# Kernel optimization log

Measured on AMD Instinct MI355X. Metric: run time of the kernel, lower is better.

The kernel has to match this reference:

```python
import jax, jax.numpy as jnp
import numpy as np

B, T, C, H, DI = 4, 1024, 1024, 16, 128
TAU = 1.0
LAMBDA_CONF = 0.1
SYS2_THR = 1.0


def _ln(x, w, b):
    mu = x.mean(-1, keepdims=True)
    var = x.var(-1, keepdims=True)
    return (x - mu) * jax.lax.rsqrt(var + 1e-5) * w + b


def setup_inputs() -> dict:
    key = jax.random.key(0)
    ks = jax.random.split(key, 16)
    s = lambda i, shape: jax.random.normal(ks[i], shape, jnp.float32) * 0.02
    return {
        "h": jax.random.normal(ks[0], (B, T, C), jnp.float32),
        "ln_w": jnp.ones((C,), jnp.float32), "ln_b": jnp.zeros((C,), jnp.float32),
        "w_q": s(1, (C, C)), "w_k": s(2, (C, C)), "w_v": s(3, (C, C)),
        "w_o": s(4, (C, C)), "b_o": jnp.zeros((C,), jnp.float32),
        "U": s(5, (C, DI)), "V": s(6, (DI, C)),
        "gamma_w": s(7, (C, 1)), "gamma_b": jnp.zeros((1,), jnp.float32),
        "mass_w": s(8, (C, 1)), "mass_b": jnp.zeros((1,), jnp.float32),
        "eps_w": s(9, (C, 1)), "eps_b": jnp.zeros((1,), jnp.float32),
        "lg_w1": s(10, (C, 4 * C)), "lg_b1": jnp.zeros((4 * C,), jnp.float32),
        "lg_w2": s(11, (4 * C, C)), "lg_b2": jnp.zeros((C,), jnp.float32),
        "mlp_w1": s(12, (C, 4 * C)), "mlp_b1": jnp.zeros((4 * C,), jnp.float32),
        "mlp_w2": s(13, (4 * C, C)), "mlp_b2": jnp.zeros((C,), jnp.float32),
    }


def reference(h, ln_w, ln_b, w_q, w_k, w_v, w_o, b_o, U, V,
              gamma_w, gamma_b, mass_w, mass_b, eps_w, eps_b,
              lg_w1, lg_b1, lg_w2, lg_b2, mlp_w1, mlp_b1, mlp_w2, mlp_b2):
    hd = C // H
    h_norm = _ln(h, ln_w, ln_b)

    # ---- HamiltonianAttention (conservative force field) ----
    q = (h_norm @ w_q).reshape(B, T, H, hd).transpose(0, 2, 1, 3)  # [B,H,T,hd]
    k = (h_norm @ w_k).reshape(B, T, H, hd).transpose(0, 2, 1, 3)
    v = (h_norm @ w_v).reshape(B, T, H, hd).transpose(0, 2, 1, 3)
    scores = jnp.einsum('bhqd,bhkd->bhqk', q, k) / (hd ** 0.5) / TAU
    attn = jax.nn.softmax(scores, axis=-1)
    force = jnp.einsum('bhqk,bhkd->bhqd', attn, v).transpose(0, 2, 1, 3).reshape(B, T, C)
    f_attn = force @ w_o + b_o

    # ---- total force, low-rank projection ----
    f_total = f_attn - LAMBDA_CONF * h_norm
    f_proj = f_total @ U                               # [B,T,DI]

    # ---- FSI (force stability index) ----
    h_mag = jnp.linalg.norm(h_norm, axis=-1)           # [B,T]
    f_mag = jnp.linalg.norm(f_proj, axis=-1)
    fsi = h_mag / (2.0 * f_mag + 1e-6)

    # ---- CognitiveGearbox: per-token mass / timestep ----
    mass = 1.0 + jax.nn.softplus(h @ mass_w + mass_b)  # [B,T,1], mass >= 1
    eps = jax.nn.sigmoid(h @ eps_w + eps_b)            # [B,T,1], eps in (0,1)
    gamma = jax.nn.sigmoid(h_norm @ gamma_w + gamma_b) # [B,T,1] damping gate

    # ---- fused AGI momentum recurrence: m_t = gamma_t*m_{t-1} + (eps_t/mass_t)*f_t ----
    def step(m, inps):
        f_t, g_t, e_t, ms_t = inps                     # [B,DI],[B,1],[B,1],[B,1]
        m = g_t * m + (e_t / ms_t) * f_t
        return m, m

    xs = (f_proj.transpose(1, 0, 2), gamma.transpose(1, 0, 2),
          eps.transpose(1, 0, 2), mass.transpose(1, 0, 2))
    m0 = jnp.zeros((B, DI), h.dtype)
    _, m_seq = jax.lax.scan(step, m0, xs)              # [T,B,DI]
    m_new = m_seq.transpose(1, 0, 2)                   # [B,T,DI]

    # ---- position update + system-2 correction + MLP ----
    velocity = m_new @ V                               # [B,T,C]
    h_new = h + eps * velocity
    hn2 = _ln(h_new, ln_w, ln_b)
    sys2 = jax.nn.gelu(hn2 @ lg_w1 + lg_b1, approximate=False) @ lg_w2 + lg_b2
    gate = jax.nn.sigmoid(mass - SYS2_THR)
    h_final = h_new + gate * sys2
    hn3 = _ln(h_final, ln_w, ln_b)
    h_final = h_final + (jax.nn.gelu(hn3 @ mlp_w1 + mlp_b1, approximate=False) @ mlp_w2 + mlp_b2)
    return (h_final, m_new, fsi)
```

## Files before the change

kernel.cpp:

```cpp
#include <hip/hip_runtime.h>
#include <hip/hip_bf16.h>
#include <math.h>

typedef __attribute__((ext_vector_type(8))) short bf16x8;
typedef __attribute__((ext_vector_type(4))) float f32x4;

#define DEVI __device__ __forceinline__

constexpr int B_ = 4, T_ = 1024, C_ = 1024, H_ = 16, HD_ = 64, DI_ = 128;
constexpr int NTOK = B_ * T_;
constexpr int C4 = 4 * C_;
constexpr int C3 = 3 * C_;
constexpr float LAMBDA_CONF = 0.1f;

DEVI short f2bf(float f) {
  unsigned u = __builtin_bit_cast(unsigned, f);
  u += 0x7fffu + ((u >> 16) & 1u);
  return (short)(u >> 16);
}
DEVI unsigned pk2(float a, float b) {
  return (unsigned)(unsigned short)f2bf(a) | ((unsigned)(unsigned short)f2bf(b) << 16);
}
DEVI float sigm(float x) { return 1.f / (1.f + __expf(-x)); }
DEVI float geluf(float x) { return 0.5f * x * (1.f + erff(x * 0.70710678118654752440f)); }

DEVI void gload16(const void* g, void* l) {
  __builtin_amdgcn_global_load_lds((const __attribute__((address_space(1))) unsigned*)g,
                                   (__attribute__((address_space(3))) unsigned*)l, 16, 0, 0);
}

template <int EPI>
DEVI void epi_store(void* Outp, const float* bias, const float* resid, const float* tokv,
                    int row, int col, int N, float v) {
  size_t idx = (size_t)row * N + col;
  if (EPI == 0) {
    ((float*)Outp)[idx] = v;
  } else if (EPI == 1) {
    ((short*)Outp)[idx] = f2bf(v);
  } else if (EPI == 2) {
    ((short*)Outp)[idx] = f2bf(v + bias[col] - LAMBDA_CONF * resid[idx]);
  } else if (EPI == 3) {
    ((float*)Outp)[idx] = resid[idx] + tokv[row] * v;
  } else if (EPI == 4) {
    float x = v + bias[col];
    ((short*)Outp)[idx] = f2bf(geluf(x));
  } else if (EPI == 5) {
    float x = v + bias[col];
    float g = sigm(tokv[row] - 1.f);
    ((float*)Outp)[idx] = resid[idx] + g * x;
  } else if (EPI == 6) {
    ((float*)Outp)[idx] = resid[idx] + v + bias[col];
  }
}

__global__ __launch_bounds__(256) void transpose_cvt(const float* __restrict__ W,
                                                     short* __restrict__ Wt, int K, int N) {
  __shared__ float s[32][33];
  int n0 = blockIdx.x * 32, k0 = blockIdx.y * 32;
  int tx = threadIdx.x & 31, ty = threadIdx.x >> 5;
#pragma unroll
  for (int i = 0; i < 4; i++)
    s[ty + i * 8][tx] = W[(size_t)(k0 + ty + i * 8) * N + n0 + tx];
  __syncthreads();
#pragma unroll
  for (int i = 0; i < 4; i++)
    Wt[(size_t)(n0 + ty + i * 8) * K + k0 + tx] = f2bf(s[tx][ty + i * 8]);
}

DEVI float blk_red(float v, volatile float* sm) {
  int lane = threadIdx.x & 63, wv = threadIdx.x >> 6;
#pragma unroll
  for (int o = 32; o; o >>= 1) v += __shfl_down(v, o);
  __syncthreads();
  if (lane == 0) sm[wv] = v;
  __syncthreads();
  return sm[0] + sm[1] + sm[2] + sm[3];
}

template <int FULL, int WF32>
__global__ __launch_bounds__(256) void ln_kernel(
    const float* __restrict__ X, const float* __restrict__ lnw, const float* __restrict__ lnb,
    float* __restrict__ Out, short* __restrict__ OutBf,
    const float* __restrict__ gw, const float* __restrict__ gb,
    const float* __restrict__ mw, const float* __restrict__ mb,
    const float* __restrict__ ew, const float* __restrict__ eb,
    float* __restrict__ gammaA, float* __restrict__ epsA, float* __restrict__ massA,
    float* __restrict__ coefA, float* __restrict__ hmagA) {
  __shared__ float sm[4];
  int tok = blockIdx.x;
  const float* x = X + (size_t)tok * C_;
  int t4 = threadIdx.x * 4;
  float4 xv = *(const float4*)&x[t4];
  float s = xv.x + xv.y + xv.z + xv.w;
  float ss = xv.x * xv.x + xv.y * xv.y + xv.z * xv.z + xv.w * xv.w;
  s = blk_red(s, sm);
  ss = blk_red(ss, sm);
  float mu = s * (1.f / C_);
  float var = ss * (1.f / C_) - mu * mu;
  float rs = rsqrtf(var + 1e-5f);
  float4 wv = *(const float4*)&lnw[t4];
  float4 bv = *(const float4*)&lnb[t4];
  float4 hn;
  hn.x = (xv.x - mu) * rs * wv.x + bv.x;
  hn.y = (xv.y - mu) * rs * wv.y + bv.y;
  hn.z = (xv.z - mu) * rs * wv.z + bv.z;
  hn.w = (xv.w - mu) * rs * wv.w + bv.w;
  if (WF32) *(float4*)&Out[(size_t)tok * C_ + t4] = hn;
  short4 ob;
  ob.x = f2bf(hn.x); ob.y = f2bf(hn.y); ob.z = f2bf(hn.z); ob.w = f2bf(hn.w);
  *(short4*)&OutBf[(size_t)tok * C_ + t4] = ob;
  if (FULL) {
    float4 gwv = *(const float4*)&gw[t4];
    float4 mwv = *(const float4*)&mw[t4];
    float4 ewv = *(const float4*)&ew[t4];
    float gd = hn.x * gwv.x + hn.y * gwv.y + hn.z * gwv.z + hn.w * gwv.w;
    float md = xv.x * mwv.x + xv.y * mwv.y + xv.z * mwv.z + xv.w * mwv.w;
    float ed = xv.x * ewv.x + xv.y * ewv.y + xv.z * ewv.z + xv.w * ewv.w;
    float h2 = hn.x * hn.x + hn.y * hn.y + hn.z * hn.z + hn.w * hn.w;
    gd = blk_red(gd, sm);
    md = blk_red(md, sm);
    ed = blk_red(ed, sm);
    h2 = blk_red(h2, sm);
    if (threadIdx.x == 0) {
      float g = sigm(gd + gb[0]);
      float xm = md + mb[0];
      float sp = (xm > 20.f) ? xm : log1pf(expf(xm));
      float msv = 1.f + sp;
      float epv = sigm(ed + eb[0]);
      gammaA[tok] = g;
      massA[tok] = msv;
      epsA[tok] = epv;
      coefA[tok] = epv / msv;
      hmagA[tok] = sqrtf(h2);
    }
  }
}

template <int EPI, int MT, int NT>
__global__ __launch_bounds__(512) void gemmP(
    const short* __restrict__ A, const short* __restrict__ Bt, void* __restrict__ Outp,
    const float* __restrict__ bias, const float* __restrict__ resid,
    const float* __restrict__ tokv, int M, int N, int K) {
  constexpr int BM = 4 * MT * 16;
  constexpr int BN = 2 * NT * 16;
  constexpr int CA = BM / 64;
  constexpr int CB = BN / 64;
  constexpr int LPT = CA + CB;
  __shared__ short As[3][BM][64];
  __shared__ short Bs[3][BN][64];
  int tid = threadIdx.x, lane = tid & 63, w = tid >> 6;
  int wr = w >> 1, wc = w & 1;
  int fr = lane & 15, fg = lane >> 4;
  int nMt = M / BM;
  int cpx = gridDim.x >> 3;
  int gbid = (blockIdx.x & 7) * cpx + (blockIdx.x >> 3);
  int chunk = gbid >> 5;
  int wi = gbid & 31;
  int nCM = nMt >> 2;
  int bm = ((chunk % nCM) * 4 + (wi & 3)) * BM;
  int bn = ((chunk / nCM) * 8 + (wi >> 2)) * BN;
  f32x4 acc[MT][NT] = {};

  int jsw = (lane & 7) ^ ((lane >> 3) & 7);
  const short* gA = A + (size_t)(bm + w * 8 + (lane >> 3)) * K + (jsw << 3);
  const short* gB = Bt + (size_t)(bn + w * 8 + (lane >> 3)) * K + (jsw << 3);

  auto stage = [&](int buf, int kt) {
#pragma unroll
    for (int c = 0; c < CA; c++)
      gload16(gA + (size_t)(c * 64) * K + kt, &As[buf][c * 64 + w * 8][0]);
#pragma unroll
    for (int c = 0; c < CB; c++)
      gload16(gB + (size_t)(c * 64) * K + kt, &Bs[buf][c * 64 + w * 8][0]);
  };

  int nt = K >> 6;
  stage(0, 0);
  if (nt > 1) stage(1, 64);
  for (int t = 0; t < nt; t++) {
    if (t + 1 < nt) {
      if constexpr (LPT == 6) asm volatile("s_waitcnt vmcnt(6)" ::: "memory");
      else asm volatile("s_waitcnt vmcnt(4)" ::: "memory");
    } else {
      asm volatile("s_waitcnt vmcnt(0)" ::: "memory");
    }
    __builtin_amdgcn_s_barrier();
    __builtin_amdgcn_sched_barrier(0);
    int nb = t + 2;
    if (nb < nt) stage(nb % 3, nb << 6);
    int cb = t % 3;
    short(*Ac)[64] = As[cb];
    short(*Bc)[64] = Bs[cb];
    bf16x8 af[MT], bv[NT / 2];
#pragma unroll
    for (int kh = 0; kh < 2; kh++) {
#pragma unroll
      for (int i = 0; i < MT; i++) {
        int row = wr * (MT * 16) + i * 16 + fr;
        af[i] = *(const bf16x8*)&Ac[row][((((kh << 2) | fg)) ^ (fr & 7)) << 3];
      }
#pragma unroll
      for (int nh = 0; nh < 2; nh++) {
#pragma unroll
        for (int j = 0; j < NT / 2; j++) {
          int row = wc * (NT * 16) + nh * (NT / 2) * 16 + j * 16 + fr;
          bv[j] = *(const bf16x8*)&Bc[row][((((kh << 2) | fg)) ^ (fr & 7)) << 3];
        }
#pragma unroll
        for (int i = 0; i < MT; i++)
#pragma unroll
          for (int j = 0; j < NT / 2; j++)
            acc[i][nh * (NT / 2) + j] = __builtin_amdgcn_mfma_f32_16x16x32_bf16(
                af[i], bv[j], acc[i][nh * (NT / 2) + j], 0, 0, 0);
      }
    }
  }

#pragma unroll
  for (int mi = 0; mi < MT; mi++) {
    int row0 = bm + wr * (MT * 16) + mi * 16 + fg * 4;
#pragma unroll
    for (int ni = 0; ni < NT; ni++) {
      int col = bn + wc * (NT * 16) + ni * 16 + fr;
#pragma unroll
      for (int r = 0; r < 4; r++)
        epi_store<EPI>(Outp, bias, resid, tokv, row0 + r, col, N, acc[mi][ni][r]);
    }
  }
}

template <int EPI>
__global__ __launch_bounds__(256) void gemm128(
    const short* __restrict__ A, const short* __restrict__ Bt, void* __restrict__ Outp,
    const float* __restrict__ bias, const float* __restrict__ resid,
    const float* __restrict__ tokv, int M, int N, int K) {
  __shared__ short As[3][128][32];
  __shared__ short Bs[3][128][32];
  int tid = threadIdx.x, lane = tid & 63, w = tid >> 6;
  int wr = w >> 1, wc = w & 1;
  int fr = lane & 15, fg = lane >> 4;
  int xm = (fr >> 1) & 3;
  int nM = M >> 7;
  int cpx = gridDim.x >> 3;
  int bid = (blockIdx.x & 7) * cpx + (blockIdx.x >> 3);
  int bm = (bid % nM) << 7;
  int bn = (bid / nM) << 7;
  f32x4 acc[4][4] = {};

  int jsw = (lane & 3) ^ ((lane >> 3) & 3);
  const short* gA = A + (size_t)(bm + w * 32 + (lane >> 2)) * K + (jsw << 3);
  const short* gB = Bt + (size_t)(bn + w * 32 + (lane >> 2)) * K + (jsw << 3);

  auto stage = [&](int buf, int kt) {
#pragma unroll
    for (int g = 0; g < 2; g++) {
      gload16(gA + (size_t)(g * 16) * K + kt, &As[buf][w * 32 + g * 16][0]);
      gload16(gB + (size_t)(g * 16) * K + kt, &Bs[buf][w * 32 + g * 16][0]);
    }
  };

  int nt = K >> 5;
  stage(0, 0);
  if (nt > 1) stage(1, 32);
  for (int t = 0; t < nt; t++) {
    if (t + 1 < nt) asm volatile("s_waitcnt vmcnt(4)" ::: "memory");
    else asm volatile("s_waitcnt vmcnt(0)" ::: "memory");
    __builtin_amdgcn_s_barrier();
    __builtin_amdgcn_sched_barrier(0);
    int nb = t + 2;
    if (nb < nt) stage(nb % 3, nb << 5);
    int cb = t % 3;
    bf16x8 af[4], bfv[4];
#pragma unroll
    for (int i = 0; i < 4; i++)
      af[i] = *(const bf16x8*)&As[cb][wr * 64 + i * 16 + fr][(fg ^ xm) << 3];
#pragma unroll
    for (int i = 0; i < 4; i++)
      bfv[i] = *(const bf16x8*)&Bs[cb][wc * 64 + i * 16 + fr][(fg ^ xm) << 3];
#pragma unroll
    for (int mi = 0; mi < 4; mi++)
#pragma unroll
      for (int ni = 0; ni < 4; ni++)
        acc[mi][ni] = __builtin_amdgcn_mfma_f32_16x16x32_bf16(af[mi], bfv[ni], acc[mi][ni], 0, 0, 0);
  }

#pragma unroll
  for (int mi = 0; mi < 4; mi++) {
    int row0 = bm + wr * 64 + mi * 16 + fg * 4;
#pragma unroll
    for (int ni = 0; ni < 4; ni++) {
      int col = bn + wc * 64 + ni * 16 + fr;
#pragma unroll
      for (int r = 0; r < 4; r++)
        epi_store<EPI>(Outp, bias, resid, tokv, row0 + r, col, N, acc[mi][ni][r]);
    }
  }
}

__global__ __launch_bounds__(256) void attn_kernel(const short* __restrict__ QKV,
                                                   short* __restrict__ Fout) {
  __shared__ short Ks[32][72];
  __shared__ short Vs[64][40];
  __shared__ short Ps[4][16][32];
  int bh = blockIdx.y;
  int b = bh >> 4, h = bh & 15;
  int qt0 = blockIdx.x * 64;
  int tid = threadIdx.x, lane = tid & 63, w = tid >> 6;
  int fr = lane & 15, fg = lane >> 4;

  size_t base = ((size_t)b * T_) * C3 + h * 64;
  const short* Qp = QKV + base;
  const short* Kp = QKV + base + C_;
  const short* Vp = QKV + base + 2 * C_;
  int qrow = qt0 + w * 16 + fr;
  bf16x8 qf0 = *(const bf16x8*)&Qp[(size_t)qrow * C3 + fg * 8];
  bf16x8 qf1 = *(const bf16x8*)&Qp[(size_t)qrow * C3 + 32 + fg * 8];

  f32x4 oacc[4] = {};
  float m_run = -1e30f, l_run = 0.f;

  int srow = tid >> 3;
  int scol = (tid & 7) * 8;

  for (int kt = 0; kt < T_; kt += 32) {
    *(uint4*)&Ks[srow][scol] = *(const uint4*)&Kp[(size_t)(kt + srow) * C3 + scol];
    {
      uint4 vv = *(const uint4*)&Vp[(size_t)(kt + srow) * C3 + scol];
      const short* sp = (const short*)&vv;
#pragma unroll
      for (int i = 0; i < 8; i++) Vs[scol + i][srow] = sp[i];
    }
    __syncthreads();

    f32x4 sacc[2];
#pragma unroll
    for (int kb = 0; kb < 2; kb++) {
      f32x4 z = {};
      bf16x8 kf0 = *(const bf16x8*)&Ks[kb * 16 + fr][fg * 8];
      bf16x8 kf1 = *(const bf16x8*)&Ks[kb * 16 + fr][32 + fg * 8];
      z = __builtin_amdgcn_mfma_f32_16x16x32_bf16(kf0, qf0, z, 0, 0, 0);
      z = __builtin_amdgcn_mfma_f32_16x16x32_bf16(kf1, qf1, z, 0, 0, 0);
      sacc[kb] = z;
    }
    float mt = -1e30f;
#pragma unroll
    for (int kb = 0; kb < 2; kb++)
#pragma unroll
      for (int r = 0; r < 4; r++) {
        sacc[kb][r] *= 0.125f;
        mt = fmaxf(mt, sacc[kb][r]);
      }
    mt = fmaxf(mt, __shfl_xor(mt, 16));
    mt = fmaxf(mt, __shfl_xor(mt, 32));
    float m_new = fmaxf(m_run, mt);
    float alpha = __expf(m_run - m_new);
    float psum = 0.f;
    float pv[8];
#pragma unroll
    for (int kb = 0; kb < 2; kb++)
#pragma unroll
      for (int r = 0; r < 4; r++) {
        float p = __expf(sacc[kb][r] - m_new);
        pv[kb * 4 + r] = p;
        psum += p;
      }
    psum += __shfl_xor(psum, 16);
    psum += __shfl_xor(psum, 32);
    l_run = l_run * alpha + psum;
    m_run = m_new;

    {
      uint2 p0, p1;
      p0.x = pk2(pv[0], pv[1]); p0.y = pk2(pv[2], pv[3]);
      p1.x = pk2(pv[4], pv[5]); p1.y = pk2(pv[6], pv[7]);
      *(uint2*)&Ps[w][fr][fg * 4] = p0;
      *(uint2*)&Ps[w][fr][16 + fg * 4] = p1;
    }
    float ar[4];
#pragma unroll
    for (int r = 0; r < 4; r++) ar[r] = __shfl(alpha, fg * 4 + r);
#pragma unroll
    for (int ni = 0; ni < 4; ni++)
#pragma unroll
      for (int r = 0; r < 4; r++) oacc[ni][r] *= ar[r];

    asm volatile("s_waitcnt lgkmcnt(0)" ::: "memory");
    bf16x8 pa = *(const bf16x8*)&Ps[w][fr][fg * 8];
#pragma unroll
    for (int ni = 0; ni < 4; ni++) {
      bf16x8 vf = *(const bf16x8*)&Vs[ni * 16 + fr][fg * 8];
      oacc[ni] = __builtin_amdgcn_mfma_f32_16x16x32_bf16(pa, vf, oacc[ni], 0, 0, 0);
    }
    __syncthreads();
  }

  float lr4[4];
#pragma unroll
  for (int r = 0; r < 4; r++) lr4[r] = __shfl(l_run, fg * 4 + r);
#pragma unroll
  for (int ni = 0; ni < 4; ni++)
#pragma unroll
    for (int r = 0; r < 4; r++) {
      int tok = b * T_ + qt0 + w * 16 + fg * 4 + r;
      Fout[(size_t)tok * C_ + h * 64 + ni * 16 + fr] = f2bf(oacc[ni][r] / lr4[r]);
    }
}

__global__ __launch_bounds__(128) void scan_kernel(const float* __restrict__ f_proj,
                                                   const float* __restrict__ gam,
                                                   const float* __restrict__ coef,
                                                   float* __restrict__ m_out,
                                                   short* __restrict__ m_bf) {
  int b = blockIdx.x;
  int d = threadIdx.x;
  const float* fp = f_proj + (size_t)b * T_ * DI_ + d;
  const float* g = gam + (size_t)b * T_;
  const float* c = coef + (size_t)b * T_;
  float* mo = m_out + (size_t)b * T_ * DI_ + d;
  short* mb = m_bf + (size_t)b * T_ * DI_ + d;
  float m = 0.f;
  for (int t = 0; t < T_; t += 8) {
    float fv[8], gv[8], cv[8];
#pragma unroll
    for (int i = 0; i < 8; i++) {
      fv[i] = fp[(size_t)(t + i) * DI_];
      gv[i] = g[t + i];
      cv[i] = c[t + i];
    }
#pragma unroll
    for (int i = 0; i < 8; i++) {
      m = gv[i] * m + cv[i] * fv[i];
      mo[(size_t)(t + i) * DI_] = m;
      mb[(size_t)(t + i) * DI_] = f2bf(m);
    }
  }
}

__global__ __launch_bounds__(256) void fsi_kernel(const float* __restrict__ f_proj,
                                                  const float* __restrict__ hmag,
                                                  float* __restrict__ fsi_out) {
  int tok = blockIdx.x * 4 + (threadIdx.x >> 6);
  int l = threadIdx.x & 63;
  float2 v = *(const float2*)&f_proj[(size_t)tok * DI_ + l * 2];
  float s = v.x * v.x + v.y * v.y;
#pragma unroll
  for (int o = 32; o; o >>= 1) s += __shfl_down(s, o);
  if (l == 0) fsi_out[tok] = hmag[tok] / (2.f * sqrtf(s) + 1e-6f);
}

extern "C" void kernel_launch(void* const* d_in, const int* in_sizes, int n_in,
                              void* d_out, int out_size, void* d_ws, size_t ws_size,
                              hipStream_t stream) {
  (void)in_sizes; (void)n_in; (void)out_size; (void)ws_size;
  const float* h = (const float*)d_in[0];
  const float* ln_w = (const float*)d_in[1];
  const float* ln_b = (const float*)d_in[2];
  const float* w_q = (const float*)d_in[3];
  const float* w_k = (const float*)d_in[4];
  const float* w_v = (const float*)d_in[5];
  const float* w_o = (const float*)d_in[6];
  const float* b_o = (const float*)d_in[7];
  const float* U = (const float*)d_in[8];
  const float* V = (const float*)d_in[9];
  const float* gamma_w = (const float*)d_in[10];
  const float* gamma_b = (const float*)d_in[11];
  const float* mass_w = (const float*)d_in[12];
  const float* mass_b = (const float*)d_in[13];
  const float* eps_w = (const float*)d_in[14];
  const float* eps_b = (const float*)d_in[15];
  const float* lg_w1 = (const float*)d_in[16];
  const float* lg_b1 = (const float*)d_in[17];
  const float* lg_w2 = (const float*)d_in[18];
  const float* lg_b2 = (const float*)d_in[19];
  const float* mlp_w1 = (const float*)d_in[20];
  const float* mlp_b1 = (const float*)d_in[21];
  const float* mlp_w2 = (const float*)d_in[22];
  const float* mlp_b2 = (const float*)d_in[23];

  float* out_h = (float*)d_out;
  float* out_m = out_h + (size_t)NTOK * C_;
  float* out_fsi = out_m + (size_t)NTOK * DI_;

  char* wsb = (char*)d_ws;
  size_t off = 0;
  auto al = [&](size_t bytes) {
    void* p = wsb + off;
    off += (bytes + 255) & ~(size_t)255;
    return p;
  };
  short* wqkvt = (short*)al((size_t)C3 * C_ * 2);
  short* wot = (short*)al((size_t)C_ * C_ * 2);
  short* ut = (short*)al((size_t)DI_ * C_ * 2);
  short* vt = (short*)al((size_t)C_ * DI_ * 2);
  short* lg1t = (short*)al((size_t)C4 * C_ * 2);
  short* lg2t = (short*)al((size_t)C_ * C4 * 2);
  short* mlp1t = (short*)al((size_t)C4 * C_ * 2);
  short* mlp2t = (short*)al((size_t)C_ * C4 * 2);
  float* h_norm = (float*)al((size_t)NTOK * C_ * 4);
  short* hn_bf = (short*)al((size_t)NTOK * C_ * 2);
  short* qkv_bf = (short*)al((size_t)NTOK * C3 * 2);
  short* tmp_bf = (short*)al((size_t)NTOK * C_ * 2);
  float* f_proj = (float*)al((size_t)NTOK * DI_ * 4);
  short* act = (short*)al((size_t)NTOK * C4 * 2);
  float* h_pre = (float*)al((size_t)NTOK * C_ * 4);
  float* gammaA = (float*)al((size_t)NTOK * 4);
  float* epsA = (float*)al((size_t)NTOK * 4);
  float* massA = (float*)al((size_t)NTOK * 4);
  float* coefA = (float*)al((size_t)NTOK * 4);
  float* hmagA = (float*)al((size_t)NTOK * 4);
  short* ftot_bf = hn_bf;
  short* m_bf = act;
  float* h_new = (float*)qkv_bf;

  dim3 blk(256);
  dim3 blk512(512);
  transpose_cvt<<<dim3(C_ / 32, C_ / 32), blk, 0, stream>>>(w_q, wqkvt, C_, C_);
  transpose_cvt<<<dim3(C_ / 32, C_ / 32), blk, 0, stream>>>(w_k, wqkvt + (size_t)C_ * C_, C_, C_);
  transpose_cvt<<<dim3(C_ / 32, C_ / 32), blk, 0, stream>>>(w_v, wqkvt + (size_t)2 * C_ * C_, C_, C_);
  transpose_cvt<<<dim3(C_ / 32, C_ / 32), blk, 0, stream>>>(w_o, wot, C_, C_);
  transpose_cvt<<<dim3(DI_ / 32, C_ / 32), blk, 0, stream>>>(U, ut, C_, DI_);
  transpose_cvt<<<dim3(C_ / 32, DI_ / 32), blk, 0, stream>>>(V, vt, DI_, C_);
  transpose_cvt<<<dim3(C4 / 32, C_ / 32), blk, 0, stream>>>(lg_w1, lg1t, C_, C4);
  transpose_cvt<<<dim3(C_ / 32, C4 / 32), blk, 0, stream>>>(lg_w2, lg2t, C4, C_);
  transpose_cvt<<<dim3(C4 / 32, C_ / 32), blk, 0, stream>>>(mlp_w1, mlp1t, C_, C4);
  transpose_cvt<<<dim3(C_ / 32, C4 / 32), blk, 0, stream>>>(mlp_w2, mlp2t, C4, C_);

  ln_kernel<1, 1><<<NTOK, blk, 0, stream>>>(h, ln_w, ln_b, h_norm, hn_bf, gamma_w, gamma_b,
                                            mass_w, mass_b, eps_w, eps_b, gammaA, epsA, massA,
                                            coefA, hmagA);
  gemmP<1, 4, 4><<<(NTOK / 256) * (C3 / 128), blk512, 0, stream>>>(hn_bf, wqkvt, qkv_bf, nullptr,
                                                                   nullptr, nullptr, NTOK, C3, C_);
  attn_kernel<<<dim3(T_ / 64, B_ * H_), blk, 0, stream>>>(qkv_bf, tmp_bf);
  gemmP<2, 2, 4><<<(NTOK / 128) * (C_ / 128), blk512, 0, stream>>>(tmp_bf, wot, ftot_bf, b_o,
                                                                   h_norm, nullptr, NTOK, C_, C_);
  gemm128<0><<<(NTOK / 128) * (DI_ / 128), blk, 0, stream>>>(ftot_bf, ut, f_proj, nullptr,
                                                             nullptr, nullptr, NTOK, DI_, C_);
  fsi_kernel<<<NTOK / 4, blk, 0, stream>>>(f_proj, hmagA, out_fsi);
  scan_kernel<<<B_, dim3(DI_), 0, stream>>>(f_proj, gammaA, coefA, out_m, m_bf);
  gemmP<3, 2, 4><<<(NTOK / 128) * (C_ / 128), blk512, 0, stream>>>(m_bf, vt, h_new, nullptr, h,
                                                                   epsA, NTOK, C_, DI_);
  ln_kernel<0, 0><<<NTOK, blk, 0, stream>>>(h_new, ln_w, ln_b, nullptr, tmp_bf, nullptr, nullptr,
                                            nullptr, nullptr, nullptr, nullptr, nullptr, nullptr,
                                            nullptr, nullptr, nullptr);
  gemmP<4, 4, 4><<<(NTOK / 256) * (C4 / 128), blk512, 0, stream>>>(tmp_bf, lg1t, act, lg_b1,
                                                                   nullptr, nullptr, NTOK, C4, C_);
  gemmP<5, 2, 4><<<(NTOK / 128) * (C_ / 128), blk512, 0, stream>>>(act, lg2t, h_pre, lg_b2,
                                                                   h_new, massA, NTOK, C_, C4);
  ln_kernel<0, 0><<<NTOK, blk, 0, stream>>>(h_pre, ln_w, ln_b, nullptr, tmp_bf, nullptr, nullptr,
                                            nullptr, nullptr, nullptr, nullptr, nullptr, nullptr,
                                            nullptr, nullptr, nullptr);
  gemmP<4, 4, 4><<<(NTOK / 256) * (C4 / 128), blk512, 0, stream>>>(tmp_bf, mlp1t, act, mlp_b1,
                                                                   nullptr, nullptr, NTOK, C4, C_);
  gemmP<6, 2, 4><<<(NTOK / 128) * (C_ / 128), blk512, 0, stream>>>(act, mlp2t, out_h, mlp_b2,
                                                                   h_pre, nullptr, NTOK, C_, C4);
}
```

Before: 578.4 us.

## Pre-transpose V and double-buffer swizzled K/V tiles in attention with async loads

Adds a separate kernel that writes V transposed per head into a scratch buffer, so the attention kernel no longer does scalar transposing stores into LDS. The attention kernel now processes 64-key tiles, loads K and V^T with direct global-to-LDS loads into XOR-swizzled double buffers, and overlaps the next tile's load with the current tile's compute. The cost is an extra launch, an extra pass over V in global memory, and more LDS per block, which may lower occupancy.

```diff
diff --git a/kernel.cpp b/kernel.cpp
--- a/kernel.cpp
+++ b/kernel.cpp
@@ -65,6 +65,23 @@
 #pragma unroll
   for (int i = 0; i < 4; i++)
     Wt[(size_t)(n0 + ty + i * 8) * K + k0 + tx] = f2bf(s[tx][ty + i * 8]);
+}
+
+__global__ __launch_bounds__(256) void transpose_v(const short* __restrict__ QKV,
+                                                   short* __restrict__ VT) {
+  __shared__ short s[32][33];
+  int bh = blockIdx.z;
+  int b = bh >> 4, h = bh & 15;
+  int t0 = blockIdx.x * 32, d0 = blockIdx.y * 32;
+  int tx = threadIdx.x & 31, ty = threadIdx.x >> 5;
+#pragma unroll
+  for (int i = 0; i < 4; i++)
+    s[ty + i * 8][tx] =
+        QKV[(size_t)(b * T_ + t0 + ty + i * 8) * C3 + 2 * C_ + h * 64 + d0 + tx];
+  __syncthreads();
+#pragma unroll
+  for (int i = 0; i < 4; i++)
+    VT[((size_t)bh * 64 + d0 + ty + i * 8) * T_ + t0 + tx] = s[tx][ty + i * 8];
 }
 
 DEVI float blk_red(float v, volatile float* sm) {
@@ -298,10 +315,11 @@
 }
 
 __global__ __launch_bounds__(256) void attn_kernel(const short* __restrict__ QKV,
+                                                   const short* __restrict__ VT,
                                                    short* __restrict__ Fout) {
-  __shared__ short Ks[32][72];
-  __shared__ short Vs[64][40];
-  __shared__ short Ps[4][16][32];
+  __shared__ short Ks[2][64][64];
+  __shared__ short Vts[2][64][64];
+  __shared__ short Ps[4][16][72];
   int bh = blockIdx.y;
   int b = bh >> 4, h = bh & 15;
   int qt0 = blockIdx.x * 64;
@@ -311,7 +329,7 @@
   size_t base = ((size_t)b * T_) * C3 + h * 64;
   const short* Qp = QKV + base;
   const short* Kp = QKV + base + C_;
-  const short* Vp = QKV + base + 2 * C_;
+  const short* Vtp = VT + (size_t)bh * 64 * T_;
   int qrow = qt0 + w * 16 + fr;
   bf16x8 qf0 = *(const bf16x8*)&Qp[(size_t)qrow * C3 + fg * 8];
   bf16x8 qf1 = *(const bf16x8*)&Qp[(size_t)qrow * C3 + 32 + fg * 8];
@@ -319,32 +337,44 @@
   f32x4 oacc[4] = {};
   float m_run = -1e30f, l_run = 0.f;
 
-  int srow = tid >> 3;
-  int scol = (tid & 7) * 8;
-
-  for (int kt = 0; kt < T_; kt += 32) {
-    *(uint4*)&Ks[srow][scol] = *(const uint4*)&Kp[(size_t)(kt + srow) * C3 + scol];
-    {
-      uint4 vv = *(const uint4*)&Vp[(size_t)(kt + srow) * C3 + scol];
-      const short* sp = (const short*)&vv;
-#pragma unroll
-      for (int i = 0; i < 8; i++) Vs[scol + i][srow] = sp[i];
-    }
-    __syncthreads();
-
-    f32x4 sacc[2];
-#pragma unroll
-    for (int kb = 0; kb < 2; kb++) {
+  int jsw = (lane & 7) ^ ((lane >> 3) & 7);
+  int sr8 = w * 8;
+  int rsub = lane >> 3;
+
+  auto stage = [&](int buf, int kt) {
+#pragma unroll
+    for (int c = 0; c < 2; c++) {
+      int row = c * 32 + sr8 + rsub;
+      gload16(Kp + (size_t)(kt + row) * C3 + jsw * 8, &Ks[buf][c * 32 + sr8][0]);
+      gload16(Vtp + (size_t)row * T_ + kt + jsw * 8, &Vts[buf][c * 32 + sr8][0]);
+    }
+  };
+
+  stage(0, 0);
+  for (int t = 0; t < T_ / 64; t++) {
+    if (t + 1 < T_ / 64) {
+      stage((t + 1) & 1, (t + 1) * 64);
+      asm volatile("s_waitcnt vmcnt(4)" ::: "memory");
+    } else {
+      asm volatile("s_waitcnt vmcnt(0)" ::: "memory");
+    }
+    __builtin_amdgcn_s_barrier();
+    __builtin_amdgcn_sched_barrier(0);
+    int cb = t & 1;
+
+    f32x4 sacc[4];
+#pragma unroll
+    for (int kb = 0; kb < 4; kb++) {
+      bf16x8 k0 = *(const bf16x8*)&Ks[cb][kb * 16 + fr][(fg ^ (fr & 7)) << 3];
+      bf16x8 k1 = *(const bf16x8*)&Ks[cb][kb * 16 + fr][((4 | fg) ^ (fr & 7)) << 3];
       f32x4 z = {};
-      bf16x8 kf0 = *(const bf16x8*)&Ks[kb * 16 + fr][fg * 8];
-      bf16x8 kf1 = *(const bf16x8*)&Ks[kb * 16 + fr][32 + fg * 8];
-      z = __builtin_amdgcn_mfma_f32_16x16x32_bf16(kf0, qf0, z, 0, 0, 0);
-      z = __builtin_amdgcn_mfma_f32_16x16x32_bf16(kf1, qf1, z, 0, 0, 0);
+      z = __builtin_amdgcn_mfma_f32_16x16x32_bf16(k0, qf0, z, 0, 0, 0);
+      z = __builtin_amdgcn_mfma_f32_16x16x32_bf16(k1, qf1, z, 0, 0, 0);
       sacc[kb] = z;
     }
     float mt = -1e30f;
 #pragma unroll
-    for (int kb = 0; kb < 2; kb++)
+    for (int kb = 0; kb < 4; kb++)
 #pragma unroll
       for (int r = 0; r < 4; r++) {
         sacc[kb][r] *= 0.125f;
@@ -355,9 +385,9 @@
     float m_new = fmaxf(m_run, mt);
     float alpha = __expf(m_run - m_new);
     float psum = 0.f;
-    float pv[8];
-#pragma unroll
-    for (int kb = 0; kb < 2; kb++)
+    float pv[16];
+#pragma unroll
+    for (int kb = 0; kb < 4; kb++)
 #pragma unroll
       for (int r = 0; r < 4; r++) {
         float p = __expf(sacc[kb][r] - m_new);
@@ -369,12 +399,12 @@
     l_run = l_run * alpha + psum;
     m_run = m_new;
 
-    {
-      uint2 p0, p1;
-      p0.x = pk2(pv[0], pv[1]); p0.y = pk2(pv[2], pv[3]);
-      p1.x = pk2(pv[4], pv[5]); p1.y = pk2(pv[6], pv[7]);
-      *(uint2*)&Ps[w][fr][fg * 4] = p0;
-      *(uint2*)&Ps[w][fr][16 + fg * 4] = p1;
+#pragma unroll
+    for (int kb = 0; kb < 4; kb++) {
+      uint2 pp;
+      pp.x = pk2(pv[kb * 4 + 0], pv[kb * 4 + 1]);
+      pp.y = pk2(pv[kb * 4 + 2], pv[kb * 4 + 3]);
+      *(uint2*)&Ps[w][fr][kb * 16 + fg * 4] = pp;
     }
     float ar[4];
 #pragma unroll
@@ -385,13 +415,17 @@
       for (int r = 0; r < 4; r++) oacc[ni][r] *= ar[r];
 
     asm volatile("s_waitcnt lgkmcnt(0)" ::: "memory");
-    bf16x8 pa = *(const bf16x8*)&Ps[w][fr][fg * 8];
+    __builtin_amdgcn_sched_barrier(0);
+    bf16x8 pa0 = *(const bf16x8*)&Ps[w][fr][fg * 8];
+    bf16x8 pa1 = *(const bf16x8*)&Ps[w][fr][32 + fg * 8];
 #pragma unroll
     for (int ni = 0; ni < 4; ni++) {
-      bf16x8 vf = *(const bf16x8*)&Vs[ni * 16 + fr][fg * 8];
-      oacc[ni] = __builtin_amdgcn_mfma_f32_16x16x32_bf16(pa, vf, oacc[ni], 0, 0, 0);
-    }
-    __syncthreads();
+      bf16x8 v0 = *(const bf16x8*)&Vts[cb][ni * 16 + fr][(fg ^ (fr & 7)) << 3];
+      bf16x8 v1 = *(const bf16x8*)&Vts[cb][ni * 16 + fr][((4 | fg) ^ (fr & 7)) << 3];
+      oacc[ni] = __builtin_amdgcn_mfma_f32_16x16x32_bf16(pa0, v0, oacc[ni], 0, 0, 0);
+      oacc[ni] = __builtin_amdgcn_mfma_f32_16x16x32_bf16(pa1, v1, oacc[ni], 0, 0, 0);
+    }
+    __builtin_amdgcn_s_barrier();
   }
 
   float lr4[4];
@@ -503,6 +537,7 @@
   float* f_proj = (float*)al((size_t)NTOK * DI_ * 4);
   short* act = (short*)al((size_t)NTOK * C4 * 2);
   float* h_pre = (float*)al((size_t)NTOK * C_ * 4);
+  short* vtrans = (short*)al((size_t)B_ * H_ * 64 * T_ * 2);
   float* gammaA = (float*)al((size_t)NTOK * 4);
   float* epsA = (float*)al((size_t)NTOK * 4);
   float* massA = (float*)al((size_t)NTOK * 4);
@@ -530,7 +565,8 @@
                                             coefA, hmagA);
   gemmP<1, 4, 4><<<(NTOK / 256) * (C3 / 128), blk512, 0, stream>>>(hn_bf, wqkvt, qkv_bf, nullptr,
                                                                    nullptr, nullptr, NTOK, C3, C_);
-  attn_kernel<<<dim3(T_ / 64, B_ * H_), blk, 0, stream>>>(qkv_bf, tmp_bf);
+  transpose_v<<<dim3(T_ / 32, 2, B_ * H_), blk, 0, stream>>>(qkv_bf, vtrans);
+  attn_kernel<<<dim3(T_ / 64, B_ * H_), blk, 0, stream>>>(qkv_bf, vtrans, tmp_bf);
   gemmP<2, 2, 4><<<(NTOK / 128) * (C_ / 128), blk512, 0, stream>>>(tmp_bf, wot, ftot_bf, b_o,
                                                                    h_norm, nullptr, NTOK, C_, C_);
   gemm128<0><<<(NTOK / 128) * (DI_ / 128), blk, 0, stream>>>(ftot_bf, ut, f_proj, nullptr,
```

Measured after the change: 540.2 us. 6.6% less time.
